# Kernel optimization log

Hardware: AMD Instinct MI355X
Metric: run time of the kernel (lower is better)

The kernel has to match this reference:

```python
import jax, jax.numpy as jnp
import numpy as np

D, NA, K, R, C = 2048, 18, 64, 10, 10
H = NA * K  # worker LSTM hidden size = n_actions * k = 1152


def _lstm_cell(x, h, c, Wih, Whh, bih, bhh):
    # torch.nn.LSTMCell gate order: i, f, g, o
    gi, gf, gg, go = jnp.split(Wih @ x + bih + Whh @ h + bhh, 4)
    c2 = jax.nn.sigmoid(gf) * c + jax.nn.sigmoid(gi) * jnp.tanh(gg)
    h2 = jax.nn.sigmoid(go) * jnp.tanh(c2)
    return h2, c2


def setup_inputs() -> dict:
    key = jax.random.key(0)
    ks = jax.random.split(key, 25)
    def n(k, shape, s=0.05):
        return jax.random.normal(k, shape, jnp.float32) * s
    return {
        'x': n(ks[0], (2,), 1.0),
        'Wp': n(ks[1], (D, 2)), 'bp': n(ks[2], (D,)),
        'Wms': n(ks[3], (D, D)), 'bms': n(ks[4], (D,)),
        'Wih_m': n(ks[5], (4 * D, D)), 'Whh_m': n(ks[6], (4 * D, D)),
        'bih_m': n(ks[7], (4 * D,)), 'bhh_m': n(ks[8], (4 * D,)),
        'hn_m': n(ks[9], (R, D)), 'cn_m': n(ks[10], (R, D)),
        'Wmv': n(ks[11], (1, D)), 'bmv': n(ks[12], (1,)),
        'Wih_w': n(ks[13], (4 * H, D)), 'Whh_w': n(ks[14], (4 * H, H)),
        'bih_w': n(ks[15], (4 * H,)), 'bhh_w': n(ks[16], (4 * H,)),
        'hn_w': n(ks[17], (H,)), 'cn_w': n(ks[18], (H,)),
        'Wphi': n(ks[19], (K, D)),
        'Wc': n(ks[20], (1, H)), 'bc': n(ks[21], (1,)),
        'states': n(ks[22], (R + 1, D)), 'goals': n(ks[23], (R, D)),
        'tick': 3,
    }


def reference(x, Wp, bp, Wms, bms, Wih_m, Whh_m, bih_m, bhh_m, hn_m, cn_m,
              Wmv, bmv, Wih_w, Whh_w, bih_w, bhh_w, hn_w, cn_w, Wphi,
              Wc, bc, states, goals, tick):
    # percept (frozen): z = relu(Linear(2, d)(x)), used as detached data
    z = jax.lax.stop_gradient(jax.nn.relu(Wp @ x + bp))

    # ----- Manager -----
    s = jax.nn.relu(Wms @ z + bms)                       # f_mspace
    h_new, _ = _lstm_cell(s, hn_m[tick], cn_m[tick], Wih_m, Whh_m, bih_m, bhh_m)
    hn2 = hn_m.at[tick].set(h_new)                       # dLSTM tick buffer
    g_hat = hn2.sum(0) / R                               # mean over ring buffer
    g = g_hat / jnp.maximum(jnp.linalg.norm(g_hat), 1e-12)  # F.normalize(dim=0)
    m_value = Wmv @ g_hat + bmv
    g_det = jax.lax.stop_gradient(g)
    s_det = jax.lax.stop_gradient(s)

    # push into fixed-size lists (already at capacity -> pop front)
    goals2 = jnp.concatenate([goals[1:], g_det[None]], axis=0)    # (R, D)
    states2 = jnp.concatenate([states[1:], s_det[None]], axis=0)  # (R+1, D)

    # ----- Worker -----
    w = Wphi @ goals2.sum(0)                             # (K,)
    u_flat, _ = _lstm_cell(z, hn_w, cn_w, Wih_w, Whh_w, bih_w, bhh_w)
    logits = u_flat.reshape(NA, K) @ w                   # Categorical logits
    w_value = Wc @ u_flat + bc

    # ----- intrinsic reward (no-grad in original) -----
    cur = states2[-1]
    diffs = cur - states2[:-1]                           # (R, D)
    num = jnp.sum(diffs * goals2, axis=1)
    den = jnp.maximum(jnp.linalg.norm(diffs, axis=1), 1e-8) * \
          jnp.maximum(jnp.linalg.norm(goals2, axis=1), 1e-8)
    cos = num / den                                      # (R,)
    # original adds scalar cosine onto a (d,)-zeros vector then sums -> factor D
    w_intrinsic_reward = jax.lax.stop_gradient(D * jnp.sum(cos) / C)

    return logits, w_intrinsic_reward, w_value, m_value
```

## Files before the change

### kernel.cpp

```cpp
#include <hip/hip_runtime.h>
#include <math.h>

#define DD 2048
#define HH 1152
#define NAA 18
#define KK 64
#define RR 10

__device__ __forceinline__ float wred(float v) {
#pragma unroll
  for (int off = 32; off > 0; off >>= 1) v += __shfl_down(v, off);
  return v;
}

__device__ __forceinline__ float sigf(float x) { return 1.f / (1.f + expf(-x)); }

__global__ void k_s(const float* __restrict__ x, const float* __restrict__ Wp,
                    const float* __restrict__ bp, const float* __restrict__ Wms,
                    const float* __restrict__ bms, float* __restrict__ s_out,
                    float* __restrict__ scal) {
  __shared__ float z[DD];
  const float x0 = x[0], x1 = x[1];
  for (int i = threadIdx.x; i < DD; i += blockDim.x) {
    float v = fmaf(Wp[2 * i], x0, fmaf(Wp[2 * i + 1], x1, bp[i]));
    z[i] = fmaxf(v, 0.f);
  }
  if (blockIdx.x == 0 && threadIdx.x < 32) scal[threadIdx.x] = 0.f;
  __syncthreads();
  const int lane = threadIdx.x & 63;
  const int gw = blockIdx.x * (blockDim.x >> 6) + (threadIdx.x >> 6);
  const int nw = gridDim.x * (blockDim.x >> 6);
  for (int row = gw; row < DD; row += nw) {
    const float4* wr = (const float4*)(Wms + (size_t)row * DD);
    float acc = 0.f;
#pragma unroll
    for (int it = 0; it < 8; ++it) {
      float4 w4 = wr[it * 64 + lane];
      float4 z4 = *(const float4*)&z[4 * (it * 64 + lane)];
      acc = fmaf(w4.x, z4.x, acc); acc = fmaf(w4.y, z4.y, acc);
      acc = fmaf(w4.z, z4.z, acc); acc = fmaf(w4.w, z4.w, acc);
    }
    acc = wred(acc);
    if (lane == 0) s_out[row] = fmaxf(acc + bms[row], 0.f);
  }
}

__global__ void k_gates(const float* __restrict__ x, const float* __restrict__ Wp,
                        const float* __restrict__ bp, const float* __restrict__ s_in,
                        const int* __restrict__ tick,
                        const float* __restrict__ Wih_m, const float* __restrict__ Whh_m,
                        const float* __restrict__ bih_m, const float* __restrict__ bhh_m,
                        const float* __restrict__ hn_m,
                        const float* __restrict__ Wih_w, const float* __restrict__ Whh_w,
                        const float* __restrict__ bih_w, const float* __restrict__ bhh_w,
                        const float* __restrict__ hn_w,
                        float* __restrict__ gates_m, float* __restrict__ gates_w) {
  __shared__ float sv[DD];
  __shared__ float zv[DD];
  __shared__ float hm[DD];
  __shared__ float hw[HH];
  const int tk = *tick;
  const float x0 = x[0], x1 = x[1];
  for (int i = threadIdx.x; i < DD; i += blockDim.x) {
    sv[i] = s_in[i];
    float v = fmaf(Wp[2 * i], x0, fmaf(Wp[2 * i + 1], x1, bp[i]));
    zv[i] = fmaxf(v, 0.f);
    hm[i] = hn_m[tk * DD + i];
  }
  for (int i = threadIdx.x; i < HH; i += blockDim.x) hw[i] = hn_w[i];
  __syncthreads();
  const int lane = threadIdx.x & 63;
  const int gw = blockIdx.x * (blockDim.x >> 6) + (threadIdx.x >> 6);
  const int nw = gridDim.x * (blockDim.x >> 6);
  const int nrows = 4 * DD + 4 * HH;
  for (int row = gw; row < nrows; row += nw) {
    if (row < 4 * DD) {
      const float4* a = (const float4*)(Wih_m + (size_t)row * DD);
      const float4* b = (const float4*)(Whh_m + (size_t)row * DD);
      float acc = 0.f;
#pragma unroll
      for (int it = 0; it < 8; ++it) {
        float4 a4 = a[it * 64 + lane];
        float4 s4 = *(const float4*)&sv[4 * (it * 64 + lane)];
        acc = fmaf(a4.x, s4.x, acc); acc = fmaf(a4.y, s4.y, acc);
        acc = fmaf(a4.z, s4.z, acc); acc = fmaf(a4.w, s4.w, acc);
        float4 b4 = b[it * 64 + lane];
        float4 h4 = *(const float4*)&hm[4 * (it * 64 + lane)];
        acc = fmaf(b4.x, h4.x, acc); acc = fmaf(b4.y, h4.y, acc);
        acc = fmaf(b4.z, h4.z, acc); acc = fmaf(b4.w, h4.w, acc);
      }
      acc = wred(acc);
      if (lane == 0) gates_m[row] = acc + bih_m[row] + bhh_m[row];
    } else {
      const int j = row - 4 * DD;
      const float4* a = (const float4*)(Wih_w + (size_t)j * DD);
      float acc = 0.f;
#pragma unroll
      for (int it = 0; it < 8; ++it) {
        float4 a4 = a[it * 64 + lane];
        float4 z4 = *(const float4*)&zv[4 * (it * 64 + lane)];
        acc = fmaf(a4.x, z4.x, acc); acc = fmaf(a4.y, z4.y, acc);
        acc = fmaf(a4.z, z4.z, acc); acc = fmaf(a4.w, z4.w, acc);
      }
      const float4* b = (const float4*)(Whh_w + (size_t)j * HH);
#pragma unroll
      for (int it = 0; it < 4; ++it) {
        float4 b4 = b[it * 64 + lane];
        float4 h4 = *(const float4*)&hw[4 * (it * 64 + lane)];
        acc = fmaf(b4.x, h4.x, acc); acc = fmaf(b4.y, h4.y, acc);
        acc = fmaf(b4.z, h4.z, acc); acc = fmaf(b4.w, h4.w, acc);
      }
      if (lane < 32) {
        float4 b4 = b[256 + lane];
        float4 h4 = *(const float4*)&hw[4 * (256 + lane)];
        acc = fmaf(b4.x, h4.x, acc); acc = fmaf(b4.y, h4.y, acc);
        acc = fmaf(b4.z, h4.z, acc); acc = fmaf(b4.w, h4.w, acc);
      }
      acc = wred(acc);
      if (lane == 0) gates_w[j] = acc + bih_w[j] + bhh_w[j];
    }
  }
}

__global__ void k_cell(const float* __restrict__ gates_m, const float* __restrict__ gates_w,
                       const int* __restrict__ tick, const float* __restrict__ hn_m,
                       const float* __restrict__ cn_m, const float* __restrict__ cn_w,
                       const float* __restrict__ Wmv, const float* __restrict__ Wc,
                       const float* __restrict__ goals, const float* __restrict__ states,
                       const float* __restrict__ s_in,
                       float* __restrict__ g_hat, float* __restrict__ goalsA,
                       float* __restrict__ u_flat, float* __restrict__ scal) {
  const int t = blockIdx.x * blockDim.x + threadIdx.x;
  const int tk = *tick;
  float r_norm2 = 0.f, r_mval = 0.f, r_wval = 0.f, r_num9h = 0.f;
  float r_dd2[10], r_num[9], r_gg2[9];
#pragma unroll
  for (int r = 0; r < 10; ++r) r_dd2[r] = 0.f;
#pragma unroll
  for (int r = 0; r < 9; ++r) { r_num[r] = 0.f; r_gg2[r] = 0.f; }

  if (t < DD) {
    const int d = t;
    float gi = gates_m[d], gf = gates_m[DD + d], gg = gates_m[2 * DD + d], go = gates_m[3 * DD + d];
    float c = cn_m[tk * DD + d];
    float c2 = sigf(gf) * c + sigf(gi) * tanhf(gg);
    float hnew = sigf(go) * tanhf(c2);
    float sum = hnew;
#pragma unroll
    for (int r = 0; r < RR; ++r) sum += (r == tk) ? 0.f : hn_m[r * DD + d];
    float gh = sum * (1.f / RR);
    g_hat[d] = gh;
    r_norm2 = gh * gh;
    r_mval = Wmv[d] * gh;
    float ga = 0.f;
    float sd = s_in[d];
#pragma unroll
    for (int r = 0; r < RR; ++r) {
      float diff = sd - states[(r + 1) * DD + d];
      r_dd2[r] = diff * diff;
      if (r < 9) {
        float gl = goals[(r + 1) * DD + d];
        ga += gl;
        r_num[r] = diff * gl;
        r_gg2[r] = gl * gl;
      } else {
        r_num9h = diff * gh;
      }
    }
    goalsA[d] = ga;
  } else if (t < DD + HH) {
    const int j = t - DD;
    float gi = gates_w[j], gf = gates_w[HH + j], gg = gates_w[2 * HH + j], go = gates_w[3 * HH + j];
    float c = cn_w[j];
    float c2 = sigf(gf) * c + sigf(gi) * tanhf(gg);
    float u = sigf(go) * tanhf(c2);
    u_flat[j] = u;
    r_wval = Wc[j] * u;
  }

  r_norm2 = wred(r_norm2); r_mval = wred(r_mval);
  r_wval = wred(r_wval);   r_num9h = wred(r_num9h);
#pragma unroll
  for (int r = 0; r < 10; ++r) r_dd2[r] = wred(r_dd2[r]);
#pragma unroll
  for (int r = 0; r < 9; ++r) { r_num[r] = wred(r_num[r]); r_gg2[r] = wred(r_gg2[r]); }
  if ((threadIdx.x & 63) == 0) {
    atomicAdd(&scal[0], r_norm2);
    atomicAdd(&scal[1], r_mval);
    atomicAdd(&scal[2], r_wval);
    atomicAdd(&scal[3], r_num9h);
#pragma unroll
    for (int r = 0; r < 10; ++r) atomicAdd(&scal[4 + r], r_dd2[r]);
#pragma unroll
    for (int r = 0; r < 9; ++r) {
      atomicAdd(&scal[14 + r], r_num[r]);
      atomicAdd(&scal[23 + r], r_gg2[r]);
    }
  }
}

__global__ void k_w(const float* __restrict__ Wphi, const float* __restrict__ g_hat,
                    const float* __restrict__ goalsA, const float* __restrict__ scal,
                    float* __restrict__ wv) {
  __shared__ float vsum[DD];
  const float rn = 1.f / fmaxf(sqrtf(scal[0]), 1e-12f);
  for (int i = threadIdx.x; i < DD; i += blockDim.x)
    vsum[i] = fmaf(g_hat[i], rn, goalsA[i]);
  __syncthreads();
  const int lane = threadIdx.x & 63;
  const int gw = blockIdx.x * (blockDim.x >> 6) + (threadIdx.x >> 6);
  if (gw < KK) {
    const float4* a = (const float4*)(Wphi + (size_t)gw * DD);
    float acc = 0.f;
#pragma unroll
    for (int it = 0; it < 8; ++it) {
      float4 a4 = a[it * 64 + lane];
      float4 v4 = *(const float4*)&vsum[4 * (it * 64 + lane)];
      acc = fmaf(a4.x, v4.x, acc); acc = fmaf(a4.y, v4.y, acc);
      acc = fmaf(a4.z, v4.z, acc); acc = fmaf(a4.w, v4.w, acc);
    }
    acc = wred(acc);
    if (lane == 0) wv[gw] = acc;
  }
}

__global__ void k_final(const float* __restrict__ u_flat, const float* __restrict__ wv,
                        const float* __restrict__ scal, const float* __restrict__ bmv,
                        const float* __restrict__ bc, float* __restrict__ out) {
  __shared__ float wl[KK];
  if (threadIdx.x < KK) wl[threadIdx.x] = wv[threadIdx.x];
  __syncthreads();
  const int lane = threadIdx.x & 63;
  const int wid = threadIdx.x >> 6;
  const int nw = blockDim.x >> 6;
  for (int a = wid; a < NAA; a += nw) {
    float acc = u_flat[a * KK + lane] * wl[lane];
    acc = wred(acc);
    if (lane == 0) out[a] = acc;
  }
  if (threadIdx.x == 0) {
    float nrm = sqrtf(scal[0]);
    float rn = 1.f / fmaxf(nrm, 1e-12f);
    float gnorm = nrm * rn;
    float csum = 0.f;
    for (int r = 0; r < 9; ++r) {
      float den = fmaxf(sqrtf(scal[4 + r]), 1e-8f) * fmaxf(sqrtf(scal[23 + r]), 1e-8f);
      csum += scal[14 + r] / den;
    }
    float den9 = fmaxf(sqrtf(scal[13]), 1e-8f) * fmaxf(gnorm, 1e-8f);
    csum += (scal[3] * rn) / den9;
    out[NAA] = (float)DD * csum / 10.f;
    out[NAA + 1] = scal[2] + bc[0];
    out[NAA + 2] = scal[1] + bmv[0];
  }
}

extern "C" void kernel_launch(void* const* d_in, const int* in_sizes, int n_in,
                              void* d_out, int out_size, void* d_ws, size_t ws_size,
                              hipStream_t stream) {
  const float* x      = (const float*)d_in[0];
  const float* Wp     = (const float*)d_in[1];
  const float* bp     = (const float*)d_in[2];
  const float* Wms    = (const float*)d_in[3];
  const float* bms    = (const float*)d_in[4];
  const float* Wih_m  = (const float*)d_in[5];
  const float* Whh_m  = (const float*)d_in[6];
  const float* bih_m  = (const float*)d_in[7];
  const float* bhh_m  = (const float*)d_in[8];
  const float* hn_m   = (const float*)d_in[9];
  const float* cn_m   = (const float*)d_in[10];
  const float* Wmv    = (const float*)d_in[11];
  const float* bmv    = (const float*)d_in[12];
  const float* Wih_w  = (const float*)d_in[13];
  const float* Whh_w  = (const float*)d_in[14];
  const float* bih_w  = (const float*)d_in[15];
  const float* bhh_w  = (const float*)d_in[16];
  const float* hn_w   = (const float*)d_in[17];
  const float* cn_w   = (const float*)d_in[18];
  const float* Wphi   = (const float*)d_in[19];
  const float* Wc     = (const float*)d_in[20];
  const float* bc     = (const float*)d_in[21];
  const float* states = (const float*)d_in[22];
  const float* goals  = (const float*)d_in[23];
  const int*   tick   = (const int*)d_in[24];

  float* ws      = (float*)d_ws;
  float* gates_m = ws;
  float* gates_w = ws + 8192;
  float* s_buf   = ws + 12800;
  float* g_hat   = ws + 14848;
  float* goalsA  = ws + 16896;
  float* u_flat  = ws + 18944;
  float* wvec    = ws + 20096;
  float* scal    = ws + 20160;
  float* out     = (float*)d_out;

  hipLaunchKernelGGL(k_s, dim3(256), dim3(256), 0, stream,
                     x, Wp, bp, Wms, bms, s_buf, scal);
  hipLaunchKernelGGL(k_gates, dim3(640), dim3(256), 0, stream,
                     x, Wp, bp, s_buf, tick,
                     Wih_m, Whh_m, bih_m, bhh_m, hn_m,
                     Wih_w, Whh_w, bih_w, bhh_w, hn_w,
                     gates_m, gates_w);
  hipLaunchKernelGGL(k_cell, dim3(13), dim3(256), 0, stream,
                     gates_m, gates_w, tick, hn_m, cn_m, cn_w, Wmv, Wc,
                     goals, states, s_buf, g_hat, goalsA, u_flat, scal);
  hipLaunchKernelGGL(k_w, dim3(16), dim3(256), 0, stream,
                     Wphi, g_hat, goalsA, scal, wvec);
  hipLaunchKernelGGL(k_final, dim3(1), dim3(512), 0, stream,
                     u_flat, wvec, scal, bmv, bc, out);
}
```

Before: 291.2 us.

## Use nontemporal weight loads, one row per wave, and fuse final kernels

Weight rows in the GEMV kernels are now read with nontemporal loads, and each wave handles exactly one row. The grids are enlarged to cover all rows (512 and 3200 blocks) instead of grid-stride loops. The Wphi projection and the final logits/scalar kernel are merged into one 1024-thread block, removing a launch and a workspace round trip. The larger grids mean each block reloads the shared vectors, adding redundant LDS fill work per block. The fused tail runs on a single CU.

```diff
diff --git a/kernel.cpp b/kernel.cpp
--- a/kernel.cpp
+++ b/kernel.cpp
@@ -7,6 +7,15 @@
 #define KK 64
 #define RR 10
 
+typedef float f32x4 __attribute__((ext_vector_type(4)));
+
+__device__ __forceinline__ f32x4 ntl4(const float* p) {
+  return __builtin_nontemporal_load((const f32x4*)p);
+}
+__device__ __forceinline__ f32x4 lds4(const float* p) {
+  return *(const f32x4*)p;
+}
+
 __device__ __forceinline__ float wred(float v) {
 #pragma unroll
   for (int off = 32; off > 0; off >>= 1) v += __shfl_down(v, off);
@@ -15,10 +24,11 @@
 
 __device__ __forceinline__ float sigf(float x) { return 1.f / (1.f + expf(-x)); }
 
-__global__ void k_s(const float* __restrict__ x, const float* __restrict__ Wp,
-                    const float* __restrict__ bp, const float* __restrict__ Wms,
-                    const float* __restrict__ bms, float* __restrict__ s_out,
-                    float* __restrict__ scal) {
+__global__ __launch_bounds__(256) void k1_s(
+    const float* __restrict__ x, const float* __restrict__ Wp,
+    const float* __restrict__ bp, const float* __restrict__ Wms,
+    const float* __restrict__ bms, float* __restrict__ s_out,
+    float* __restrict__ scal) {
   __shared__ float z[DD];
   const float x0 = x[0], x1 = x[1];
   for (int i = threadIdx.x; i < DD; i += blockDim.x) {
@@ -28,33 +38,32 @@
   if (blockIdx.x == 0 && threadIdx.x < 32) scal[threadIdx.x] = 0.f;
   __syncthreads();
   const int lane = threadIdx.x & 63;
-  const int gw = blockIdx.x * (blockDim.x >> 6) + (threadIdx.x >> 6);
-  const int nw = gridDim.x * (blockDim.x >> 6);
-  for (int row = gw; row < DD; row += nw) {
-    const float4* wr = (const float4*)(Wms + (size_t)row * DD);
-    float acc = 0.f;
-#pragma unroll
-    for (int it = 0; it < 8; ++it) {
-      float4 w4 = wr[it * 64 + lane];
-      float4 z4 = *(const float4*)&z[4 * (it * 64 + lane)];
-      acc = fmaf(w4.x, z4.x, acc); acc = fmaf(w4.y, z4.y, acc);
-      acc = fmaf(w4.z, z4.z, acc); acc = fmaf(w4.w, z4.w, acc);
-    }
-    acc = wred(acc);
-    if (lane == 0) s_out[row] = fmaxf(acc + bms[row], 0.f);
-  }
-}
-
-__global__ void k_gates(const float* __restrict__ x, const float* __restrict__ Wp,
-                        const float* __restrict__ bp, const float* __restrict__ s_in,
-                        const int* __restrict__ tick,
-                        const float* __restrict__ Wih_m, const float* __restrict__ Whh_m,
-                        const float* __restrict__ bih_m, const float* __restrict__ bhh_m,
-                        const float* __restrict__ hn_m,
-                        const float* __restrict__ Wih_w, const float* __restrict__ Whh_w,
-                        const float* __restrict__ bih_w, const float* __restrict__ bhh_w,
-                        const float* __restrict__ hn_w,
-                        float* __restrict__ gates_m, float* __restrict__ gates_w) {
+  const int row = blockIdx.x * 4 + (threadIdx.x >> 6);
+  if (row >= DD) return;
+  const float* a = Wms + (size_t)row * DD;
+  float acc = 0.f;
+#pragma unroll
+  for (int it = 0; it < 8; ++it) {
+    f32x4 w4 = ntl4(a + 4 * (it * 64 + lane));
+    f32x4 z4 = lds4(&z[4 * (it * 64 + lane)]);
+    acc = fmaf(w4[0], z4[0], acc); acc = fmaf(w4[1], z4[1], acc);
+    acc = fmaf(w4[2], z4[2], acc); acc = fmaf(w4[3], z4[3], acc);
+  }
+  acc = wred(acc);
+  if (lane == 0) s_out[row] = fmaxf(acc + bms[row], 0.f);
+}
+
+__global__ __launch_bounds__(256) void k2_gates(
+    const float* __restrict__ x, const float* __restrict__ Wp,
+    const float* __restrict__ bp, const float* __restrict__ s_in,
+    const int* __restrict__ tick,
+    const float* __restrict__ Wih_m, const float* __restrict__ Whh_m,
+    const float* __restrict__ bih_m, const float* __restrict__ bhh_m,
+    const float* __restrict__ hn_m,
+    const float* __restrict__ Wih_w, const float* __restrict__ Whh_w,
+    const float* __restrict__ bih_w, const float* __restrict__ bhh_w,
+    const float* __restrict__ hn_w,
+    float* __restrict__ gates_m, float* __restrict__ gates_w) {
   __shared__ float sv[DD];
   __shared__ float zv[DD];
   __shared__ float hm[DD];
@@ -70,66 +79,66 @@
   for (int i = threadIdx.x; i < HH; i += blockDim.x) hw[i] = hn_w[i];
   __syncthreads();
   const int lane = threadIdx.x & 63;
-  const int gw = blockIdx.x * (blockDim.x >> 6) + (threadIdx.x >> 6);
-  const int nw = gridDim.x * (blockDim.x >> 6);
-  const int nrows = 4 * DD + 4 * HH;
-  for (int row = gw; row < nrows; row += nw) {
-    if (row < 4 * DD) {
-      const float4* a = (const float4*)(Wih_m + (size_t)row * DD);
-      const float4* b = (const float4*)(Whh_m + (size_t)row * DD);
-      float acc = 0.f;
-#pragma unroll
-      for (int it = 0; it < 8; ++it) {
-        float4 a4 = a[it * 64 + lane];
-        float4 s4 = *(const float4*)&sv[4 * (it * 64 + lane)];
-        acc = fmaf(a4.x, s4.x, acc); acc = fmaf(a4.y, s4.y, acc);
-        acc = fmaf(a4.z, s4.z, acc); acc = fmaf(a4.w, s4.w, acc);
-        float4 b4 = b[it * 64 + lane];
-        float4 h4 = *(const float4*)&hm[4 * (it * 64 + lane)];
-        acc = fmaf(b4.x, h4.x, acc); acc = fmaf(b4.y, h4.y, acc);
-        acc = fmaf(b4.z, h4.z, acc); acc = fmaf(b4.w, h4.w, acc);
-      }
-      acc = wred(acc);
-      if (lane == 0) gates_m[row] = acc + bih_m[row] + bhh_m[row];
-    } else {
-      const int j = row - 4 * DD;
-      const float4* a = (const float4*)(Wih_w + (size_t)j * DD);
-      float acc = 0.f;
-#pragma unroll
-      for (int it = 0; it < 8; ++it) {
-        float4 a4 = a[it * 64 + lane];
-        float4 z4 = *(const float4*)&zv[4 * (it * 64 + lane)];
-        acc = fmaf(a4.x, z4.x, acc); acc = fmaf(a4.y, z4.y, acc);
-        acc = fmaf(a4.z, z4.z, acc); acc = fmaf(a4.w, z4.w, acc);
-      }
-      const float4* b = (const float4*)(Whh_w + (size_t)j * HH);
-#pragma unroll
-      for (int it = 0; it < 4; ++it) {
-        float4 b4 = b[it * 64 + lane];
-        float4 h4 = *(const float4*)&hw[4 * (it * 64 + lane)];
-        acc = fmaf(b4.x, h4.x, acc); acc = fmaf(b4.y, h4.y, acc);
-        acc = fmaf(b4.z, h4.z, acc); acc = fmaf(b4.w, h4.w, acc);
-      }
-      if (lane < 32) {
-        float4 b4 = b[256 + lane];
-        float4 h4 = *(const float4*)&hw[4 * (256 + lane)];
-        acc = fmaf(b4.x, h4.x, acc); acc = fmaf(b4.y, h4.y, acc);
-        acc = fmaf(b4.z, h4.z, acc); acc = fmaf(b4.w, h4.w, acc);
-      }
-      acc = wred(acc);
-      if (lane == 0) gates_w[j] = acc + bih_w[j] + bhh_w[j];
-    }
-  }
-}
-
-__global__ void k_cell(const float* __restrict__ gates_m, const float* __restrict__ gates_w,
-                       const int* __restrict__ tick, const float* __restrict__ hn_m,
-                       const float* __restrict__ cn_m, const float* __restrict__ cn_w,
-                       const float* __restrict__ Wmv, const float* __restrict__ Wc,
-                       const float* __restrict__ goals, const float* __restrict__ states,
-                       const float* __restrict__ s_in,
-                       float* __restrict__ g_hat, float* __restrict__ goalsA,
-                       float* __restrict__ u_flat, float* __restrict__ scal) {
+  const int row = blockIdx.x * 4 + (threadIdx.x >> 6);
+  if (row < 4 * DD) {
+    const float* a = Wih_m + (size_t)row * DD;
+    const float* b = Whh_m + (size_t)row * DD;
+    float acc = 0.f;
+#pragma unroll
+    for (int it = 0; it < 8; ++it) {
+      f32x4 a4 = ntl4(a + 4 * (it * 64 + lane));
+      f32x4 s4 = lds4(&sv[4 * (it * 64 + lane)]);
+      acc = fmaf(a4[0], s4[0], acc); acc = fmaf(a4[1], s4[1], acc);
+      acc = fmaf(a4[2], s4[2], acc); acc = fmaf(a4[3], s4[3], acc);
+    }
+#pragma unroll
+    for (int it = 0; it < 8; ++it) {
+      f32x4 b4 = ntl4(b + 4 * (it * 64 + lane));
+      f32x4 h4 = lds4(&hm[4 * (it * 64 + lane)]);
+      acc = fmaf(b4[0], h4[0], acc); acc = fmaf(b4[1], h4[1], acc);
+      acc = fmaf(b4[2], h4[2], acc); acc = fmaf(b4[3], h4[3], acc);
+    }
+    acc = wred(acc);
+    if (lane == 0) gates_m[row] = acc + bih_m[row] + bhh_m[row];
+  } else {
+    const int j = row - 4 * DD;
+    if (j >= 4 * HH) return;
+    const float* a = Wih_w + (size_t)j * DD;
+    const float* b = Whh_w + (size_t)j * HH;
+    float acc = 0.f;
+#pragma unroll
+    for (int it = 0; it < 8; ++it) {
+      f32x4 a4 = ntl4(a + 4 * (it * 64 + lane));
+      f32x4 z4 = lds4(&zv[4 * (it * 64 + lane)]);
+      acc = fmaf(a4[0], z4[0], acc); acc = fmaf(a4[1], z4[1], acc);
+      acc = fmaf(a4[2], z4[2], acc); acc = fmaf(a4[3], z4[3], acc);
+    }
+#pragma unroll
+    for (int it = 0; it < 4; ++it) {
+      f32x4 b4 = ntl4(b + 4 * (it * 64 + lane));
+      f32x4 h4 = lds4(&hw[4 * (it * 64 + lane)]);
+      acc = fmaf(b4[0], h4[0], acc); acc = fmaf(b4[1], h4[1], acc);
+      acc = fmaf(b4[2], h4[2], acc); acc = fmaf(b4[3], h4[3], acc);
+    }
+    if (lane < 32) {
+      f32x4 b4 = ntl4(b + 4 * (256 + lane));
+      f32x4 h4 = lds4(&hw[4 * (256 + lane)]);
+      acc = fmaf(b4[0], h4[0], acc); acc = fmaf(b4[1], h4[1], acc);
+      acc = fmaf(b4[2], h4[2], acc); acc = fmaf(b4[3], h4[3], acc);
+    }
+    acc = wred(acc);
+    if (lane == 0) gates_w[j] = acc + bih_w[j] + bhh_w[j];
+  }
+}
+
+__global__ void k3_cell(const float* __restrict__ gates_m, const float* __restrict__ gates_w,
+                        const int* __restrict__ tick, const float* __restrict__ hn_m,
+                        const float* __restrict__ cn_m, const float* __restrict__ cn_w,
+                        const float* __restrict__ Wmv, const float* __restrict__ Wc,
+                        const float* __restrict__ goals, const float* __restrict__ states,
+                        const float* __restrict__ s_in,
+                        float* __restrict__ g_hat, float* __restrict__ goalsA,
+                        float* __restrict__ u_flat, float* __restrict__ scal) {
   const int t = blockIdx.x * blockDim.x + threadIdx.x;
   const int tk = *tick;
   float r_norm2 = 0.f, r_mval = 0.f, r_wval = 0.f, r_num9h = 0.f;
@@ -199,56 +208,51 @@
   }
 }
 
-__global__ void k_w(const float* __restrict__ Wphi, const float* __restrict__ g_hat,
-                    const float* __restrict__ goalsA, const float* __restrict__ scal,
-                    float* __restrict__ wv) {
+__global__ __launch_bounds__(1024) void k4_wf(
+    const float* __restrict__ Wphi, const float* __restrict__ g_hat,
+    const float* __restrict__ goalsA, const float* __restrict__ u_flat,
+    const float* __restrict__ scal, const float* __restrict__ bmv,
+    const float* __restrict__ bc, float* __restrict__ out) {
   __shared__ float vsum[DD];
+  __shared__ float wl[KK];
   const float rn = 1.f / fmaxf(sqrtf(scal[0]), 1e-12f);
   for (int i = threadIdx.x; i < DD; i += blockDim.x)
     vsum[i] = fmaf(g_hat[i], rn, goalsA[i]);
   __syncthreads();
   const int lane = threadIdx.x & 63;
-  const int gw = blockIdx.x * (blockDim.x >> 6) + (threadIdx.x >> 6);
-  if (gw < KK) {
-    const float4* a = (const float4*)(Wphi + (size_t)gw * DD);
+  const int wid = threadIdx.x >> 6;
+#pragma unroll
+  for (int i = 0; i < 4; ++i) {
+    const int row = wid * 4 + i;
+    const float* a = Wphi + (size_t)row * DD;
     float acc = 0.f;
 #pragma unroll
     for (int it = 0; it < 8; ++it) {
-      float4 a4 = a[it * 64 + lane];
-      float4 v4 = *(const float4*)&vsum[4 * (it * 64 + lane)];
-      acc = fmaf(a4.x, v4.x, acc); acc = fmaf(a4.y, v4.y, acc);
-      acc = fmaf(a4.z, v4.z, acc); acc = fmaf(a4.w, v4.w, acc);
+      f32x4 a4 = lds4(a + 4 * (it * 64 + lane));
+      f32x4 v4 = lds4(&vsum[4 * (it * 64 + lane)]);
+      acc = fmaf(a4[0], v4[0], acc); acc = fmaf(a4[1], v4[1], acc);
+      acc = fmaf(a4[2], v4[2], acc); acc = fmaf(a4[3], v4[3], acc);
     }
     acc = wred(acc);
-    if (lane == 0) wv[gw] = acc;
-  }
-}
-
-__global__ void k_final(const float* __restrict__ u_flat, const float* __restrict__ wv,
-                        const float* __restrict__ scal, const float* __restrict__ bmv,
-                        const float* __restrict__ bc, float* __restrict__ out) {
-  __shared__ float wl[KK];
-  if (threadIdx.x < KK) wl[threadIdx.x] = wv[threadIdx.x];
+    if (lane == 0) wl[row] = acc;
+  }
   __syncthreads();
-  const int lane = threadIdx.x & 63;
-  const int wid = threadIdx.x >> 6;
-  const int nw = blockDim.x >> 6;
-  for (int a = wid; a < NAA; a += nw) {
+  for (int a = wid; a < NAA; a += 16) {
     float acc = u_flat[a * KK + lane] * wl[lane];
     acc = wred(acc);
     if (lane == 0) out[a] = acc;
   }
   if (threadIdx.x == 0) {
     float nrm = sqrtf(scal[0]);
-    float rn = 1.f / fmaxf(nrm, 1e-12f);
-    float gnorm = nrm * rn;
+    float rnn = 1.f / fmaxf(nrm, 1e-12f);
+    float gnorm = nrm * rnn;
     float csum = 0.f;
     for (int r = 0; r < 9; ++r) {
       float den = fmaxf(sqrtf(scal[4 + r]), 1e-8f) * fmaxf(sqrtf(scal[23 + r]), 1e-8f);
       csum += scal[14 + r] / den;
     }
     float den9 = fmaxf(sqrtf(scal[13]), 1e-8f) * fmaxf(gnorm, 1e-8f);
-    csum += (scal[3] * rn) / den9;
+    csum += (scal[3] * rnn) / den9;
     out[NAA] = (float)DD * csum / 10.f;
     out[NAA + 1] = scal[2] + bc[0];
     out[NAA + 2] = scal[1] + bmv[0];
@@ -291,22 +295,19 @@
   float* g_hat   = ws + 14848;
   float* goalsA  = ws + 16896;
   float* u_flat  = ws + 18944;
-  float* wvec    = ws + 20096;
   float* scal    = ws + 20160;
   float* out     = (float*)d_out;
 
-  hipLaunchKernelGGL(k_s, dim3(256), dim3(256), 0, stream,
+  hipLaunchKernelGGL(k1_s, dim3(512), dim3(256), 0, stream,
                      x, Wp, bp, Wms, bms, s_buf, scal);
-  hipLaunchKernelGGL(k_gates, dim3(640), dim3(256), 0, stream,
+  hipLaunchKernelGGL(k2_gates, dim3(3200), dim3(256), 0, stream,
                      x, Wp, bp, s_buf, tick,
                      Wih_m, Whh_m, bih_m, bhh_m, hn_m,
                      Wih_w, Whh_w, bih_w, bhh_w, hn_w,
                      gates_m, gates_w);
-  hipLaunchKernelGGL(k_cell, dim3(13), dim3(256), 0, stream,
+  hipLaunchKernelGGL(k3_cell, dim3(13), dim3(256), 0, stream,
                      gates_m, gates_w, tick, hn_m, cn_m, cn_w, Wmv, Wc,
                      goals, states, s_buf, g_hat, goalsA, u_flat, scal);
-  hipLaunchKernelGGL(k_w, dim3(16), dim3(256), 0, stream,
-                     Wphi, g_hat, goalsA, scal, wvec);
-  hipLaunchKernelGGL(k_final, dim3(1), dim3(512), 0, stream,
-                     u_flat, wvec, scal, bmv, bc, out);
-}
+  hipLaunchKernelGGL(k4_wf, dim3(1), dim3(1024), 0, stream,
+                     Wphi, g_hat, goalsA, u_flat, scal, bmv, bc, out);
+}
```

New measurement: 275.1 us. -5.5%, faster.
